# Kernel optimization log

Hardware: AMD Instinct MI355X
Metric: run time of the kernel (lower is better)

## Reference

```python
import jax, jax.numpy as jnp
import numpy as np

H, C = 4, 32  # heads, per-head channels
EPS = 1e-5


def setup_inputs() -> dict:
    key = jax.random.key(0)
    ks = jax.random.split(key, 12)
    N, E, IN = 100000, 1600000, 16
    lut_idx = jnp.arange(1024, dtype=jnp.int32)
    x = jax.random.normal(ks[0], (N, IN), dtype=jnp.float32)
    # LUT flag column: exactly the lut_idx nodes have value 1.0 (matches x[:,15]==1.0 mask)
    x = x.at[:, 15].set(0.0).at[lut_idx, 15].set(1.0)
    edge_index = jax.random.randint(ks[1], (2, E), 0, N, dtype=jnp.int64)
    s = 0.1
    return {
        "x": x,
        "edge_index": edge_index,
        "lut_idx": lut_idx,
        "W_lin": jax.random.normal(ks[2], (IN, H * C), dtype=jnp.float32) * s,
        "att_src": jax.random.normal(ks[3], (H, C), dtype=jnp.float32) * s,
        "att_dst": jax.random.normal(ks[4], (H, C), dtype=jnp.float32) * s,
        "bias_gat": jnp.zeros((H * C,), dtype=jnp.float32),
        "gamma": jnp.ones((H * C,), dtype=jnp.float32),
        "beta": jnp.zeros((H * C,), dtype=jnp.float32),
        "W1": jax.random.normal(ks[5], (H * C, 32), dtype=jnp.float32) * s,
        "b1": jnp.zeros((32,), dtype=jnp.float32),
        "W2": jax.random.normal(ks[6], (32, 1), dtype=jnp.float32) * s,
        "b2": jnp.zeros((1,), dtype=jnp.float32),
    }


def gat_conv(x, edge_index, W_lin, att_src, att_dst, bias_gat):
    N = x.shape[0]
    # add self-loops (PyG GATConv default)
    loops = jnp.arange(N, dtype=edge_index.dtype)
    src = jnp.concatenate([edge_index[0], loops])
    dst = jnp.concatenate([edge_index[1], loops])
    h = (x @ W_lin).reshape(N, H, C)                      # [N,H,C]
    a_src = (h * att_src[None]).sum(-1)                   # [N,H]
    a_dst = (h * att_dst[None]).sum(-1)                   # [N,H]
    e = jax.nn.leaky_relu(a_src[src] + a_dst[dst], 0.2)   # [Etot,H]
    m = jax.ops.segment_max(e, dst, num_segments=N)       # stable softmax per dst
    e = jnp.exp(e - m[dst])
    denom = jax.ops.segment_sum(e, dst, num_segments=N)
    alpha = e / denom[dst]                                # [Etot,H]
    msg = h[src] * alpha[:, :, None]                      # [Etot,H,C]
    out = jax.ops.segment_sum(msg, dst, num_segments=N)   # [N,H,C]
    return out.reshape(N, H * C) + bias_gat


def reference(x, edge_index, lut_idx, W_lin, att_src, att_dst, bias_gat,
              gamma, beta, W1, b1, W2, b2):
    h = gat_conv(x, edge_index, W_lin, att_src, att_dst, bias_gat)
    # BatchNorm over nodes (training-mode batch stats, biased var, eps=1e-5)
    mean = h.mean(axis=0)
    var = h.var(axis=0)
    h = (h - mean) / jnp.sqrt(var + EPS) * gamma + beta
    h = jax.nn.relu(h)
    emb = h[lut_idx]                                      # masked LUT nodes
    z = jax.nn.leaky_relu(emb @ W1 + b1, 0.01)            # Dropout is identity in eval
    out = z @ W2 + b2                                     # [n_lut, 1]
    return jnp.squeeze(out, axis=0) if out.shape[0] == 1 else out
```

## Files before the change

### kernel.cpp

```cpp
#include <hip/hip_runtime.h>
#include <hip/hip_fp16.h>
#include <cstdint>
#include <cstring>

typedef unsigned int uint;

#define BSHIFT 8
#define NBUCK 512
#define TILE 4096
#define FUSE_T 1024
#define LS_T 512
#define SORT_CAP 5120

__device__ __forceinline__ float leaky02(float x) { return x > 0.f ? x : 0.2f * x; }
__device__ __forceinline__ float bflo(uint u) { return __uint_as_float(u << 16); }
__device__ __forceinline__ float bfhi(uint u) { return __uint_as_float(u & 0xffff0000u); }

__device__ __forceinline__ uint pack_bf16x2(float a, float b) {
    uint ua = __float_as_uint(a), ub = __float_as_uint(b);
    ua += 0x7fffu + ((ua >> 16) & 1u);
    ub += 0x7fffu + ((ub >> 16) & 1u);
    return (ua >> 16) | (ub & 0xffff0000u);
}

__device__ __forceinline__ uint packh2(float a, float b) {
    __half ha = __float2half_rn(a), hb = __float2half_rn(b);
    unsigned short ua, ub;
    memcpy(&ua, &ha, 2);
    memcpy(&ub, &hb, 2);
    return (uint)ua | ((uint)ub << 16);
}

__device__ __forceinline__ float h2f_sel(uint2 xw, int head) {
    uint wrd = (head & 2) ? xw.y : xw.x;
    unsigned short us = (unsigned short)((head & 1) ? (wrd >> 16) : (wrd & 0xffffu));
    __half hh; memcpy(&hh, &us, 2);
    return __half2float(hh);
}

__global__ void k_linscat(const float* __restrict__ x, const float* __restrict__ W,
                          const float* __restrict__ att_s, const float* __restrict__ att_d,
                          uint* __restrict__ h, float* __restrict__ a_src,
                          float* __restrict__ a_dst,
                          const int* __restrict__ src, const int* __restrict__ dst, int E,
                          int* __restrict__ cursor, uint* __restrict__ pairs,
                          const int* __restrict__ lut, int nlut,
                          unsigned char* __restrict__ flags, int N, int Lb) {
    int tid = threadIdx.x;
    if (blockIdx.x < Lb) {
        __shared__ float sx[64][16];
        __shared__ float sWs[64], sWd[64];
        int j = tid & 63;
        int sub = tid >> 6;
        int n0 = blockIdx.x * 64;

        float2 wreg[16];
#pragma unroll
        for (int k = 0; k < 16; k++) wreg[k] = ((const float2*)(W + k * 128))[j];

        if (tid < 256) {
            int row = tid >> 2;
            if (n0 + row < N)
                ((float4*)sx)[tid] = ((const float4*)(x + (size_t)n0 * 16))[tid];
        } else if (tid < 320) {
            int t = tid - 256;
            int k = t >> 2, hh = t & 3;
            float s1 = 0.f, s2 = 0.f;
            for (int c = 0; c < 32; c++) {
                float wv = W[k * 128 + hh * 32 + c];
                s1 += wv * att_s[hh * 32 + c];
                s2 += wv * att_d[hh * 32 + c];
            }
            sWs[t] = s1;
            sWd[t] = s2;
        }
        __syncthreads();

#pragma unroll
        for (int i = 0; i < 8; i++) {
            int loc = sub + i * 8;
            int n = n0 + loc;
            if (n >= N) break;
            float acc0 = 0.f, acc1 = 0.f;
#pragma unroll
            for (int k = 0; k < 16; k++) {
                float xk = sx[loc][k];
                acc0 += xk * wreg[k].x;
                acc1 += xk * wreg[k].y;
            }
            h[(size_t)n * 64 + j] = pack_bf16x2(acc0, acc1);
        }

        int loc2 = tid >> 3, hh = (tid >> 1) & 3, sd = tid & 1;
        int n2 = n0 + loc2;
        if (n2 < N) {
            const float* Wm = sd ? sWd : sWs;
            float acc = 0.f;
#pragma unroll
            for (int k = 0; k < 16; k++) acc += sx[loc2][k] * Wm[k * 4 + hh];
            if (sd) a_dst[n2 * 4 + hh] = acc;
            else    a_src[n2 * 4 + hh] = acc;
        }
    } else {
        __shared__ int tileCnt[NBUCK], tileCnt2[NBUCK], gbase[NBUCK];
        int bid = blockIdx.x - Lb;
        int t0 = bid * TILE;
        if (bid == 0) {
            for (int k = tid; k < nlut; k += LS_T) flags[lut[k]] = 1;
        }
        tileCnt[tid] = 0;
        tileCnt2[tid] = 0;
        __syncthreads();
        int dreg[8], sreg[8];
#pragma unroll
        for (int jj = 0; jj < 8; jj++) {
            int idx = t0 + jj * LS_T + tid;
            if (idx < E) {
                dreg[jj] = dst[idx];
                sreg[jj] = src[idx];
                atomicAdd(&tileCnt[dreg[jj] >> BSHIFT], 1);
            } else dreg[jj] = -1;
        }
        __syncthreads();
        int v = tileCnt[tid];
        if (v > 0) gbase[tid] = atomicAdd(&cursor[tid], v);
        __syncthreads();
#pragma unroll
        for (int jj = 0; jj < 8; jj++) {
            if (dreg[jj] >= 0) {
                int bk = dreg[jj] >> BSHIFT;
                int r = atomicAdd(&tileCnt2[bk], 1);
                int pos = gbase[bk] + r;
                if (pos < SORT_CAP)
                    pairs[(size_t)bk * SORT_CAP + pos] =
                        ((uint)sreg[jj] << BSHIFT) | (uint)(dreg[jj] & 255);
            }
        }
    }
}

__global__ void __launch_bounds__(1024, 8) kb_sortgat(
                           const uint* __restrict__ pairs, const int* __restrict__ cursor,
                           const float* __restrict__ a_src, const float* __restrict__ a_dst,
                           const uint* __restrict__ h, const float* __restrict__ bias,
                           const unsigned char* __restrict__ flags,
                           uint* __restrict__ hagg,
                           float* __restrict__ sums, float* __restrict__ sumsq, int N) {
    __shared__ int cnt[256], off0[256], degl[256];
    __shared__ int wsum[4], wbase[4];
    __shared__ uint lcode[SORT_CAP];
    __shared__ uint2 wlds[SORT_CAP];
    __shared__ float4 sad[256];
    __shared__ float4 sbias[32];
    int tid = threadIdx.x;
    int l = tid & 63, w = tid >> 6;
    int b = blockIdx.x;
    int n0 = b << BSHIFT;
    int nn = min(256, N - n0);
    int ebase = b * SORT_CAP;
    int ecnt = cursor[b];
    if (ecnt > SORT_CAP) ecnt = SORT_CAP;
    if (tid < 256) cnt[tid] = 0;
    if (tid < nn) sad[tid] = ((const float4*)a_dst)[n0 + tid];
    if (tid >= 992) sbias[tid - 992] = ((const float4*)bias)[tid - 992];
    __syncthreads();
    for (int k = tid; k < ecnt; k += FUSE_T)
        atomicAdd(&cnt[pairs[ebase + k] & 255], 1);
    __syncthreads();
    int v = (tid < 256) ? cnt[tid] : 0;
    int s = v;
#pragma unroll
    for (int off = 1; off < 64; off <<= 1) {
        int t = __shfl_up(s, off);
        if (l >= off) s += t;
    }
    if (tid < 256 && l == 63) wsum[w] = s;
    __syncthreads();
    if (tid < 4) {
        int base = 0;
        for (int i = 0; i < tid; i++) base += wsum[i];
        wbase[tid] = base;
    }
    __syncthreads();
    if (tid < 256) {
        off0[tid] = s - v + wbase[w];
        degl[tid] = v;
    }
    __syncthreads();
    if (tid < 256) cnt[tid] = 0;
    __syncthreads();
    for (int k = tid; k < ecnt; k += FUSE_T) {
        uint p = pairs[ebase + k];
        int ln = p & 255;
        int src = (int)(p >> BSHIFT);
        int r = atomicAdd(&cnt[ln], 1);
        int pos = off0[ln] + r;
        lcode[pos] = (uint)src;
        float4 as = ((const float4*)a_src)[src];
        float4 ad = sad[ln];
        wlds[pos] = make_uint2(
            packh2(__expf(leaky02(as.x + ad.x)), __expf(leaky02(as.y + ad.y))),
            packh2(__expf(leaky02(as.z + ad.z)), __expf(leaky02(as.w + ad.w))));
    }
    __syncthreads();
    int q = l >> 4;
    int l16 = l & 15;
    int head = l16 >> 2;
    float sv[8], sq[8];
#pragma unroll
    for (int j = 0; j < 8; j++) { sv[j] = 0.f; sq[j] = 0.f; }
    for (int pass = 0; pass < 4; pass++) {
        int ln = pass * 64 + w * 4 + q;
        if (ln >= nn) continue;
        int d = n0 + ln;
        int ebs = off0[ln];
        int deg = degl[ln];
        float asv = a_src[d * 4 + head];
        float adv = ((const float*)sad)[ln * 4 + head];
        float wslf = __expf(leaky02(asv + adv));
        uint4 u = ((const uint4*)(h + (size_t)d * 64))[l16];
        float sum = wslf;
        float2 a01 = make_float2(wslf * bflo(u.x), wslf * bfhi(u.x));
        float2 a23 = make_float2(wslf * bflo(u.y), wslf * bfhi(u.y));
        float2 a45 = make_float2(wslf * bflo(u.z), wslf * bfhi(u.z));
        float2 a67 = make_float2(wslf * bflo(u.w), wslf * bfhi(u.w));

        int i = 0;
        for (; i + 1 < deg; i += 2) {
            uint p0 = lcode[ebs + i];
            uint p1 = lcode[ebs + i + 1];
            float w0 = h2f_sel(wlds[ebs + i], head);
            float w1 = h2f_sel(wlds[ebs + i + 1], head);
            uint4 u0 = ((const uint4*)(h + (size_t)p0 * 64))[l16];
            uint4 u1 = ((const uint4*)(h + (size_t)p1 * 64))[l16];
            sum += w0 + w1;
            float2 w02 = {w0, w0}, w12 = {w1, w1};
            a01 += make_float2(bflo(u0.x), bfhi(u0.x)) * w02
                 + make_float2(bflo(u1.x), bfhi(u1.x)) * w12;
            a23 += make_float2(bflo(u0.y), bfhi(u0.y)) * w02
                 + make_float2(bflo(u1.y), bfhi(u1.y)) * w12;
            a45 += make_float2(bflo(u0.z), bfhi(u0.z)) * w02
                 + make_float2(bflo(u1.z), bfhi(u1.z)) * w12;
            a67 += make_float2(bflo(u0.w), bfhi(u0.w)) * w02
                 + make_float2(bflo(u1.w), bfhi(u1.w)) * w12;
        }
        if (i < deg) {
            uint p0 = lcode[ebs + i];
            float w0 = h2f_sel(wlds[ebs + i], head);
            uint4 u0 = ((const uint4*)(h + (size_t)p0 * 64))[l16];
            sum += w0;
            float2 w02 = {w0, w0};
            a01 += make_float2(bflo(u0.x), bfhi(u0.x)) * w02;
            a23 += make_float2(bflo(u0.y), bfhi(u0.y)) * w02;
            a45 += make_float2(bflo(u0.z), bfhi(u0.z)) * w02;
            a67 += make_float2(bflo(u0.w), bfhi(u0.w)) * w02;
        }
        float inv = 1.f / sum;
        float4 b0 = sbias[2 * l16];
        float4 b1 = sbias[2 * l16 + 1];
        float v0 = a01.x * inv + b0.x;
        float v1 = a01.y * inv + b0.y;
        float v2 = a23.x * inv + b0.z;
        float v3 = a23.y * inv + b0.w;
        float v4 = a45.x * inv + b1.x;
        float v5 = a45.y * inv + b1.y;
        float v6 = a67.x * inv + b1.z;
        float v7 = a67.y * inv + b1.w;
        sv[0] += v0; sq[0] += v0 * v0;
        sv[1] += v1; sq[1] += v1 * v1;
        sv[2] += v2; sq[2] += v2 * v2;
        sv[3] += v3; sq[3] += v3 * v3;
        sv[4] += v4; sq[4] += v4 * v4;
        sv[5] += v5; sq[5] += v5 * v5;
        sv[6] += v6; sq[6] += v6 * v6;
        sv[7] += v7; sq[7] += v7 * v7;
        if (flags[d]) {
            uint4 o;
            o.x = pack_bf16x2(v0, v1);
            o.y = pack_bf16x2(v2, v3);
            o.z = pack_bf16x2(v4, v5);
            o.w = pack_bf16x2(v6, v7);
            ((uint4*)(hagg + (size_t)d * 64))[l16] = o;
        }
    }
    __syncthreads();
#pragma unroll
    for (int j = 0; j < 8; j++) {
        sv[j] += __shfl_xor(sv[j], 16);
        sv[j] += __shfl_xor(sv[j], 32);
        sq[j] += __shfl_xor(sq[j], 16);
        sq[j] += __shfl_xor(sq[j], 32);
    }
    float* red = (float*)lcode;
    if (l < 16) {
#pragma unroll
        for (int j = 0; j < 8; j++) {
            red[(w * 16 + l) * 16 + j] = sv[j];
            red[(w * 16 + l) * 16 + 8 + j] = sq[j];
        }
    }
    __syncthreads();
    if (tid < 256) {
        int lg = tid >> 4, j = tid & 15;
        float tot = 0.f;
#pragma unroll
        for (int ww = 0; ww < 16; ww++) tot += red[(ww * 16 + lg) * 16 + j];
        if (j < 8) atomicAdd(&sums[lg * 8 + j], tot);
        else       atomicAdd(&sumsq[lg * 8 + j - 8], tot);
    }
}

__global__ void k_mlp(const uint* __restrict__ hagg, const int* __restrict__ lut,
                      const float* __restrict__ sums, const float* __restrict__ sumsq,
                      const float* __restrict__ gamma, const float* __restrict__ beta,
                      const float* __restrict__ W1, const float* __restrict__ b1,
                      const float* __restrict__ W2, const float* __restrict__ b2,
                      float* __restrict__ out, int N, int nlut) {
    int blk = blockIdx.x;
    if (blk >= nlut) return;
    int node = lut[blk];
    int lane = threadIdx.x;
    __shared__ float v[128];
    float invN = 1.f / (float)N;
    uint u = hagg[(size_t)node * 64 + lane];
    int c0 = 2 * lane, c1 = 2 * lane + 1;
    {
        float mean = sums[c0] * invN;
        float var = sumsq[c0] * invN - mean * mean;
        float val = (bflo(u) - mean) / sqrtf(var + 1e-5f) * gamma[c0] + beta[c0];
        v[c0] = fmaxf(val, 0.f);
        mean = sums[c1] * invN;
        var = sumsq[c1] * invN - mean * mean;
        val = (bfhi(u) - mean) / sqrtf(var + 1e-5f) * gamma[c1] + beta[c1];
        v[c1] = fmaxf(val, 0.f);
    }
    __syncthreads();
    float r = 0.f;
    if (lane < 32) {
        float z = b1[lane];
        for (int c = 0; c < 128; c++) z += v[c] * W1[c * 32 + lane];
        z = z > 0.f ? z : 0.01f * z;
        r = z * W2[lane];
    }
#pragma unroll
    for (int off = 16; off >= 1; off >>= 1) r += __shfl_xor(r, off);
    if (lane == 0) out[blk] = r + b2[0];
}

extern "C" void kernel_launch(void* const* d_in, const int* in_sizes, int n_in,
                              void* d_out, int out_size, void* d_ws, size_t ws_size,
                              hipStream_t stream) {
    const float* x     = (const float*)d_in[0];
    const int*   edges = (const int*)d_in[1];
    const int*   lut   = (const int*)d_in[2];
    const float* W_lin = (const float*)d_in[3];
    const float* att_s = (const float*)d_in[4];
    const float* att_d = (const float*)d_in[5];
    const float* bias  = (const float*)d_in[6];
    const float* gamma = (const float*)d_in[7];
    const float* beta  = (const float*)d_in[8];
    const float* W1    = (const float*)d_in[9];
    const float* b1    = (const float*)d_in[10];
    const float* W2    = (const float*)d_in[11];
    const float* b2    = (const float*)d_in[12];

    int N = in_sizes[0] / 16;
    int E = in_sizes[1] / 2;
    int nlut = in_sizes[2];
    int B = (N + 255) >> BSHIFT;
    int Lb = (N + 63) / 64;
    int Sb = (E + TILE - 1) / TILE;

    const int* esrc = edges;
    const int* edst = edges + E;

    char* ws = (char*)d_ws;
    size_t off = 0;
    auto alloc = [&](size_t bytes) -> void* {
        void* p = ws + off;
        off += (bytes + 255) & ~(size_t)255;
        return p;
    };
    uint*  h       = (uint*)alloc((size_t)N * 64 * 4);
    uint*  hagg    = (uint*)alloc((size_t)N * 64 * 4);
    float* a_src   = (float*)alloc((size_t)N * 4 * 4);
    float* a_dst   = (float*)alloc((size_t)N * 4 * 4);
    uint*  pairs   = (uint*)alloc((size_t)B * SORT_CAP * 4);
    char*  zbase   = ws + off;
    int*   cursor  = (int*)alloc((size_t)NBUCK * 4);
    float* sums    = (float*)alloc(128 * 4);
    float* sumsq   = (float*)alloc(128 * 4);
    unsigned char* flags = (unsigned char*)alloc((size_t)N);
    size_t zspan = (size_t)((ws + off) - zbase);

    hipMemsetAsync(zbase, 0, zspan, stream);
    k_linscat<<<Lb + Sb, LS_T, 0, stream>>>(x, W_lin, att_s, att_d, h, a_src, a_dst,
                                            esrc, edst, E, cursor, pairs,
                                            lut, nlut, flags, N, Lb);
    kb_sortgat<<<B, FUSE_T, 0, stream>>>(pairs, cursor, a_src, a_dst, h, bias,
                                         flags, hagg, sums, sumsq, N);
    k_mlp<<<nlut, 64, 0, stream>>>(hagg, lut, sums, sumsq, gamma, beta, W1, b1, W2, b2,
                                   (float*)d_out, N, nlut);
}
```

Baseline: 192.7 us.

## Fuse LUT MLP into aggregation kernel via last-block-done pattern

```diff
diff --git a/kernel.cpp b/kernel.cpp
--- a/kernel.cpp
+++ b/kernel.cpp
@@ -44,8 +44,7 @@
                           float* __restrict__ a_dst,
                           const int* __restrict__ src, const int* __restrict__ dst, int E,
                           int* __restrict__ cursor, uint* __restrict__ pairs,
-                          const int* __restrict__ lut, int nlut,
-                          unsigned char* __restrict__ flags, int N, int Lb) {
+                          int N, int Lb) {
     int tid = threadIdx.x;
     if (blockIdx.x < Lb) {
         __shared__ float sx[64][16];
@@ -105,9 +104,6 @@
         __shared__ int tileCnt[NBUCK], tileCnt2[NBUCK], gbase[NBUCK];
         int bid = blockIdx.x - Lb;
         int t0 = bid * TILE;
-        if (bid == 0) {
-            for (int k = tid; k < nlut; k += LS_T) flags[lut[k]] = 1;
-        }
         tileCnt[tid] = 0;
         tileCnt2[tid] = 0;
         __syncthreads();
@@ -143,15 +139,21 @@
                            const uint* __restrict__ pairs, const int* __restrict__ cursor,
                            const float* __restrict__ a_src, const float* __restrict__ a_dst,
                            const uint* __restrict__ h, const float* __restrict__ bias,
-                           const unsigned char* __restrict__ flags,
                            uint* __restrict__ hagg,
-                           float* __restrict__ sums, float* __restrict__ sumsq, int N) {
+                           float* __restrict__ sums, float* __restrict__ sumsq,
+                           int* __restrict__ done,
+                           const int* __restrict__ lut, int nlut,
+                           const float* __restrict__ gamma, const float* __restrict__ beta,
+                           const float* __restrict__ W1, const float* __restrict__ b1,
+                           const float* __restrict__ W2, const float* __restrict__ b2,
+                           float* __restrict__ out, int N) {
     __shared__ int cnt[256], off0[256], degl[256];
     __shared__ int wsum[4], wbase[4];
     __shared__ uint lcode[SORT_CAP];
     __shared__ uint2 wlds[SORT_CAP];
     __shared__ float4 sad[256];
     __shared__ float4 sbias[32];
+    __shared__ int lastFlag;
     int tid = threadIdx.x;
     int l = tid & 63, w = tid >> 6;
     int b = blockIdx.x;
@@ -257,15 +259,15 @@
         }
         float inv = 1.f / sum;
         float4 b0 = sbias[2 * l16];
-        float4 b1 = sbias[2 * l16 + 1];
+        float4 b1v = sbias[2 * l16 + 1];
         float v0 = a01.x * inv + b0.x;
         float v1 = a01.y * inv + b0.y;
         float v2 = a23.x * inv + b0.z;
         float v3 = a23.y * inv + b0.w;
-        float v4 = a45.x * inv + b1.x;
-        float v5 = a45.y * inv + b1.y;
-        float v6 = a67.x * inv + b1.z;
-        float v7 = a67.y * inv + b1.w;
+        float v4 = a45.x * inv + b1v.x;
+        float v5 = a45.y * inv + b1v.y;
+        float v6 = a67.x * inv + b1v.z;
+        float v7 = a67.y * inv + b1v.w;
         sv[0] += v0; sq[0] += v0 * v0;
         sv[1] += v1; sq[1] += v1 * v1;
         sv[2] += v2; sq[2] += v2 * v2;
@@ -274,7 +276,7 @@
         sv[5] += v5; sq[5] += v5 * v5;
         sv[6] += v6; sq[6] += v6 * v6;
         sv[7] += v7; sq[7] += v7 * v7;
-        if (flags[d]) {
+        {
             uint4 o;
             o.x = pack_bf16x2(v0, v1);
             o.y = pack_bf16x2(v2, v3);
@@ -308,43 +310,70 @@
         if (j < 8) atomicAdd(&sums[lg * 8 + j], tot);
         else       atomicAdd(&sumsq[lg * 8 + j - 8], tot);
     }
-}
-
-__global__ void k_mlp(const uint* __restrict__ hagg, const int* __restrict__ lut,
-                      const float* __restrict__ sums, const float* __restrict__ sumsq,
-                      const float* __restrict__ gamma, const float* __restrict__ beta,
-                      const float* __restrict__ W1, const float* __restrict__ b1,
-                      const float* __restrict__ W2, const float* __restrict__ b2,
-                      float* __restrict__ out, int N, int nlut) {
-    int blk = blockIdx.x;
-    if (blk >= nlut) return;
-    int node = lut[blk];
-    int lane = threadIdx.x;
-    __shared__ float v[128];
+    __syncthreads();
+    __threadfence();
+    if (tid == 0) {
+        int old = atomicAdd(done, 1);
+        lastFlag = (old == (int)gridDim.x - 1);
+    }
+    __syncthreads();
+    if (!lastFlag) return;
+    __threadfence();
+    float* w1s  = (float*)wlds;
+    float* sgam = w1s + 4096;
+    float* sbet = sgam + 128;
+    float* sb1  = sbet + 128;
+    float* sw2  = sb1 + 32;
+    float* smean= sw2 + 32;
+    float* svar = smean + 128;
+    float* vbuf = (float*)lcode;
+    for (int k = tid; k < 4096; k += FUSE_T) w1s[k] = W1[k];
     float invN = 1.f / (float)N;
-    uint u = hagg[(size_t)node * 64 + lane];
-    int c0 = 2 * lane, c1 = 2 * lane + 1;
-    {
-        float mean = sums[c0] * invN;
-        float var = sumsq[c0] * invN - mean * mean;
-        float val = (bflo(u) - mean) / sqrtf(var + 1e-5f) * gamma[c0] + beta[c0];
-        v[c0] = fmaxf(val, 0.f);
-        mean = sums[c1] * invN;
-        var = sumsq[c1] * invN - mean * mean;
-        val = (bfhi(u) - mean) / sqrtf(var + 1e-5f) * gamma[c1] + beta[c1];
-        v[c1] = fmaxf(val, 0.f);
-    }
-    __syncthreads();
-    float r = 0.f;
-    if (lane < 32) {
-        float z = b1[lane];
-        for (int c = 0; c < 128; c++) z += v[c] * W1[c * 32 + lane];
-        z = z > 0.f ? z : 0.01f * z;
-        r = z * W2[lane];
-    }
-#pragma unroll
-    for (int off = 16; off >= 1; off >>= 1) r += __shfl_xor(r, off);
-    if (lane == 0) out[blk] = r + b2[0];
+    if (tid < 128) {
+        sgam[tid] = gamma[tid];
+        sbet[tid] = beta[tid];
+        float sm = atomicAdd(&sums[tid], 0.f);
+        float s2 = atomicAdd(&sumsq[tid], 0.f);
+        float mean = sm * invN;
+        smean[tid] = mean;
+        svar[tid] = s2 * invN - mean * mean;
+    } else if (tid < 160) {
+        sb1[tid - 128] = b1[tid - 128];
+        sw2[tid - 128] = W2[tid - 128];
+    }
+    __syncthreads();
+    float b2v = b2[0];
+    int lane2 = l & 31, half = l >> 5;
+    float* v0p = vbuf + w * 256;
+    float* v1p = v0p + 128;
+    for (int base = 0; base < nlut; base += 32) {
+        int i0 = base + 2 * w;
+        if (i0 < nlut) {
+            int nd = lut[i0];
+            uint uu = hagg[(size_t)nd * 64 + l];
+            int c0 = 2 * l, c1 = c0 + 1;
+            v0p[c0] = fmaxf((bflo(uu) - smean[c0]) / sqrtf(svar[c0] + 1e-5f) * sgam[c0] + sbet[c0], 0.f);
+            v0p[c1] = fmaxf((bfhi(uu) - smean[c1]) / sqrtf(svar[c1] + 1e-5f) * sgam[c1] + sbet[c1], 0.f);
+        }
+        if (i0 + 1 < nlut) {
+            int nd = lut[i0 + 1];
+            uint uu = hagg[(size_t)nd * 64 + l];
+            int c0 = 2 * l, c1 = c0 + 1;
+            v1p[c0] = fmaxf((bflo(uu) - smean[c0]) / sqrtf(svar[c0] + 1e-5f) * sgam[c0] + sbet[c0], 0.f);
+            v1p[c1] = fmaxf((bfhi(uu) - smean[c1]) / sqrtf(svar[c1] + 1e-5f) * sgam[c1] + sbet[c1], 0.f);
+        }
+        int idx = i0 + half;
+        if (idx < nlut) {
+            const float* vv = half ? v1p : v0p;
+            float z = sb1[lane2];
+            for (int c = 0; c < 128; c++) z += vv[c] * w1s[c * 32 + lane2];
+            z = z > 0.f ? z : 0.01f * z;
+            float r = z * sw2[lane2];
+#pragma unroll
+            for (int off2 = 16; off2 >= 1; off2 >>= 1) r += __shfl_xor(r, off2, 32);
+            if (lane2 == 0) out[idx] = r + b2v;
+        }
+    }
 }
 
 extern "C" void kernel_launch(void* const* d_in, const int* in_sizes, int n_in,
@@ -390,15 +419,14 @@
     int*   cursor  = (int*)alloc((size_t)NBUCK * 4);
     float* sums    = (float*)alloc(128 * 4);
     float* sumsq   = (float*)alloc(128 * 4);
-    unsigned char* flags = (unsigned char*)alloc((size_t)N);
+    int*   done    = (int*)alloc(256);
     size_t zspan = (size_t)((ws + off) - zbase);
 
     hipMemsetAsync(zbase, 0, zspan, stream);
     k_linscat<<<Lb + Sb, LS_T, 0, stream>>>(x, W_lin, att_s, att_d, h, a_src, a_dst,
-                                            esrc, edst, E, cursor, pairs,
-                                            lut, nlut, flags, N, Lb);
+                                            esrc, edst, E, cursor, pairs, N, Lb);
     kb_sortgat<<<B, FUSE_T, 0, stream>>>(pairs, cursor, a_src, a_dst, h, bias,
-                                         flags, hagg, sums, sumsq, N);
-    k_mlp<<<nlut, 64, 0, stream>>>(hagg, lut, sums, sumsq, gamma, beta, W1, b1, W2, b2,
-                                   (float*)d_out, N, nlut);
-}
+                                         hagg, sums, sumsq, done, lut, nlut,
+                                         gamma, beta, W1, b1, W2, b2,
+                                         (float*)d_out, N);
+}
```

Result: slower. 449.6 us (+133.3%).
